# Kernel tuning notes

Measured on AMD Instinct MI355X. Metric: run time of the kernel, lower is better.

Reference implementation:

```python
import jax, jax.numpy as jnp
import numpy as np

N, E = 50000, 800000          # nodes, edges
H, C = 4, 64                  # heads, out_channels
F_IN, F_E = 5, 1              # node feature dim, edge feature dim
NEG_SLOPE = 0.2               # PyG GATConv default LeakyReLU slope
EPS = 1e-16                   # PyG softmax denominator epsilon


def setup_inputs() -> dict:
    key = jax.random.key(0)
    ks = jax.random.split(key, 10)
    return {
        "x": jax.random.normal(ks[0], (N, F_IN), jnp.float32),
        "edge_attr": jax.random.normal(ks[1], (E, F_E), jnp.float32),
        "u": jax.random.normal(ks[2], (1, 1), jnp.float32),
        # learned params (glorot-ish scale)
        "W": jax.random.normal(ks[3], (F_IN, H * C), jnp.float32) * 0.3,
        "W_edge": jax.random.normal(ks[4], (F_E, H * C), jnp.float32) * 0.3,
        "att_src": jax.random.normal(ks[5], (H, C), jnp.float32) * 0.1,
        "att_dst": jax.random.normal(ks[6], (H, C), jnp.float32) * 0.1,
        "att_edge": jax.random.normal(ks[7], (H, C), jnp.float32) * 0.1,
        "bias": jnp.zeros((C,), jnp.float32),
        "edge_index": jax.random.randint(ks[8], (2, E), 0, N, dtype=jnp.int32),
        "batch": jnp.zeros((N,), jnp.int32),
    }


def reference(x, edge_attr, u, W, W_edge, att_src, att_dst, att_edge, bias,
              edge_index, batch):
    # dropout p=0.0 is identity; u and batch are unused by the module's forward.
    src, dst = edge_index[0], edge_index[1]

    # node transform: [N, H, C]
    h = (x @ W).reshape(-1, H, C)
    # per-node attention logits: [N, H]
    a_src = jnp.einsum("nhc,hc->nh", h, att_src)
    a_dst = jnp.einsum("nhc,hc->nh", h, att_dst)

    # edge transform + edge attention logits: [E, H]
    e = (edge_attr @ W_edge).reshape(-1, H, C)
    a_edge = jnp.einsum("ehc,hc->eh", e, att_edge)

    # per-edge logits, LeakyReLU: [E, H]
    alpha = jax.nn.leaky_relu(a_src[src] + a_dst[dst] + a_edge, NEG_SLOPE)

    # segment softmax grouped by destination node
    m = jax.ops.segment_max(alpha, dst, num_segments=N)        # [N, H]
    alpha = jnp.exp(alpha - m[dst])
    s = jax.ops.segment_sum(alpha, dst, num_segments=N)        # [N, H]
    alpha = alpha / (s[dst] + EPS)

    # weighted scatter-aggregate of source features: [N, H, C]
    msg = h[src] * alpha[:, :, None]                           # [E, H, C]
    out = jax.ops.segment_sum(msg, dst, num_segments=N)

    # concat=False -> mean over heads, then bias: [N, C]
    return out.mean(axis=1) + bias
```

## Files before the change

kernel.cpp:

```cpp
#include <hip/hip_runtime.h>
#include <hip/hip_fp16.h>

#define N_NODES 50000
#define N_EDGES 800000
#define NH 4
#define NC 64
#define HC 256
#define F_IN 5
#define NEG_SLOPE 0.2f
#define SM_EPS 1e-16f
#define CAP 64
#define EPT 4
#define NPB 64
#define PREP_BLOCKS ((N_NODES + 255) / 256)
#define PLACE_BLOCKS ((N_EDGES + 256 * EPT - 1) / (256 * EPT))
#define GO_GRID ((N_NODES + NPB - 1) / NPB)

__device__ __forceinline__ float wave_reduce_sum(float v) {
#pragma unroll
    for (int o = 32; o > 0; o >>= 1) v += __shfl_xor(v, o, 64);
    return v;
}

__global__ __launch_bounds__(256) void prep_place_kernel(
        const float* __restrict__ x, const float* __restrict__ W,
        const float* __restrict__ att_src, const float* __restrict__ att_dst,
        const int* __restrict__ ei, const float* __restrict__ edge_attr,
        float* __restrict__ nrec, int* __restrict__ cursor,
        unsigned int* __restrict__ rec) {
    const int t = threadIdx.x;
    if (blockIdx.x < PREP_BLOCKS) {
        __shared__ float Vs[F_IN][NH], Vd[F_IN][NH];
        const int head = t >> 6, lane = t & 63;
        const float asv = att_src[t], adv = att_dst[t];
#pragma unroll
        for (int f = 0; f < F_IN; ++f) {
            const float w = W[f * HC + t];
            float vs = wave_reduce_sum(w * asv);
            float vd = wave_reduce_sum(w * adv);
            if (lane == 0) { Vs[f][head] = vs; Vd[f][head] = vd; }
        }
        __syncthreads();

        const int n = blockIdx.x * 256 + t;
        if (n >= N_NODES) return;
        float xs[F_IN];
#pragma unroll
        for (int f = 0; f < F_IN; ++f) xs[f] = x[n * F_IN + f];
        float as[NH] = {0.f, 0.f, 0.f, 0.f}, ad[NH] = {0.f, 0.f, 0.f, 0.f};
#pragma unroll
        for (int f = 0; f < F_IN; ++f)
#pragma unroll
            for (int h = 0; h < NH; ++h) {
                as[h] += xs[f] * Vs[f][h];
                ad[h] += xs[f] * Vd[f][h];
            }
        float* r = nrec + (size_t)n * 16;
        ((float4*)r)[0] = make_float4(as[0], as[1], as[2], as[3]);
        ((float4*)r)[1] = make_float4(xs[0], xs[1], xs[2], xs[3]);
        ((float4*)r)[2] = make_float4(xs[4], 0.f, 0.f, 0.f);
        ((float4*)r)[3] = make_float4(ad[0], ad[1], ad[2], ad[3]);
    } else {
        const int pb = blockIdx.x - PREP_BLOCKS;
        const int e0 = (pb * 256 + t) * EPT;
        if (e0 >= N_EDGES) return;
        if (e0 + EPT <= N_EDGES) {
            const int4 s4 = *(const int4*)(ei + e0);
            const int4 d4 = *(const int4*)(ei + N_EDGES + e0);
            const float4 a4 = *(const float4*)(edge_attr + e0);
            const int ss[EPT] = {s4.x, s4.y, s4.z, s4.w};
            const int dd[EPT] = {d4.x, d4.y, d4.z, d4.w};
            const float aa[EPT] = {a4.x, a4.y, a4.z, a4.w};
            int slot[EPT];
#pragma unroll
            for (int k = 0; k < EPT; ++k) slot[k] = atomicAdd(&cursor[dd[k]], 1);
#pragma unroll
            for (int k = 0; k < EPT; ++k) {
                if (slot[k] < CAP) {
                    const unsigned int h16 =
                        (unsigned int)__half_as_ushort(__float2half(aa[k]));
                    rec[(size_t)dd[k] * CAP + slot[k]] =
                        ((unsigned int)ss[k] << 16) | h16;
                }
            }
        } else {
            for (int e = e0; e < N_EDGES; ++e) {
                const int src = ei[e];
                const int dst = ei[N_EDGES + e];
                const int slot = atomicAdd(&cursor[dst], 1);
                if (slot < CAP) {
                    const unsigned int h16 =
                        (unsigned int)__half_as_ushort(__float2half(edge_attr[e]));
                    rec[(size_t)dst * CAP + slot] = ((unsigned int)src << 16) | h16;
                }
            }
        }
    }
}

__global__ __launch_bounds__(256) void gatherout_kernel(
        const float* __restrict__ W_edge, const float* __restrict__ att_edge,
        const int* __restrict__ cursor, const unsigned int* __restrict__ rec,
        const float* __restrict__ nrec, const float* __restrict__ W,
        const float* __restrict__ bias, float* __restrict__ out) {
    __shared__ float aeS[NH];
    __shared__ float nacc[NPB][21];
    const int t = threadIdx.x;
    {
        const int head = t >> 6, lane = t & 63;
        float v = wave_reduce_sum(W_edge[t] * att_edge[t]);
        if (lane == 0) aeS[head] = v;
    }
    __syncthreads();
    const float ae0 = aeS[0], ae1 = aeS[1], ae2 = aeS[2], ae3 = aeS[3];

    const int nl = t >> 2, parity = t & 3;
    const int n = blockIdx.x * NPB + nl;

    float acc[NH][F_IN];
#pragma unroll
    for (int h = 0; h < NH; ++h)
#pragma unroll
        for (int f = 0; f < F_IN; ++f) acc[h][f] = 0.f;
    float sden[NH] = {0.f, 0.f, 0.f, 0.f};

    if (n < N_NODES) {
        int cnt = cursor[n];
        cnt = cnt < CAP ? cnt : CAP;
        const float4 ad = ((const float4*)(nrec + (size_t)n * 16))[3];
        const unsigned int* rp = rec + (size_t)n * CAP;
        for (int i = parity; i < cnt; i += 4) {
            const unsigned int r = rp[i];
            const int src = (int)(r >> 16);
            const float ea = __half2float(__ushort_as_half((unsigned short)(r & 0xffffu)));
            const float* sr = nrec + (size_t)src * 16;
            const float4 as = ((const float4*)sr)[0];
            const float4 xa = ((const float4*)sr)[1];
            const float x4v = sr[8];
            float l0 = as.x + ad.x + ea * ae0;
            float l1 = as.y + ad.y + ea * ae1;
            float l2 = as.z + ad.z + ea * ae2;
            float l3 = as.w + ad.w + ea * ae3;
            l0 = l0 > 0.f ? l0 : NEG_SLOPE * l0;
            l1 = l1 > 0.f ? l1 : NEG_SLOPE * l1;
            l2 = l2 > 0.f ? l2 : NEG_SLOPE * l2;
            l3 = l3 > 0.f ? l3 : NEG_SLOPE * l3;
            const float p0 = expf(l0), p1 = expf(l1), p2 = expf(l2), p3 = expf(l3);
            const float xs[F_IN] = {xa.x, xa.y, xa.z, xa.w, x4v};
            const float pv[NH] = {p0, p1, p2, p3};
#pragma unroll
            for (int h = 0; h < NH; ++h) {
                sden[h] += pv[h];
#pragma unroll
                for (int f = 0; f < F_IN; ++f) acc[h][f] += pv[h] * xs[f];
            }
        }
    }
#pragma unroll
    for (int h = 0; h < NH; ++h) {
        sden[h] += __shfl_xor(sden[h], 1, 64);
        sden[h] += __shfl_xor(sden[h], 2, 64);
#pragma unroll
        for (int f = 0; f < F_IN; ++f) {
            acc[h][f] += __shfl_xor(acc[h][f], 1, 64);
            acc[h][f] += __shfl_xor(acc[h][f], 2, 64);
        }
    }
    if (parity == 0 && n < N_NODES) {
#pragma unroll
        for (int h = 0; h < NH; ++h) {
            const float is = 0.25f / (sden[h] + SM_EPS);
#pragma unroll
            for (int f = 0; f < F_IN; ++f) nacc[nl][h * F_IN + f] = acc[h][f] * is;
        }
    }
    __syncthreads();

    const int c = t & 63;
    float wreg[NH][F_IN];
#pragma unroll
    for (int h = 0; h < NH; ++h)
#pragma unroll
        for (int f = 0; f < F_IN; ++f) wreg[h][f] = W[f * HC + h * NC + c];
    const float bv = bias[c];
#pragma unroll
    for (int k = 0; k < NPB / 4; ++k) {
        const int nl2 = k * 4 + (t >> 6);
        const int n2 = blockIdx.x * NPB + nl2;
        if (n2 < N_NODES) {
            float r = bv;
#pragma unroll
            for (int h = 0; h < NH; ++h)
#pragma unroll
                for (int f = 0; f < F_IN; ++f)
                    r += nacc[nl2][h * F_IN + f] * wreg[h][f];
            out[(size_t)n2 * NC + c] = r;
        }
    }
}

extern "C" void kernel_launch(void* const* d_in, const int* in_sizes, int n_in,
                              void* d_out, int out_size, void* d_ws, size_t ws_size,
                              hipStream_t stream) {
    const float* x         = (const float*)d_in[0];
    const float* edge_attr = (const float*)d_in[1];
    const float* W         = (const float*)d_in[3];
    const float* W_edge    = (const float*)d_in[4];
    const float* att_src   = (const float*)d_in[5];
    const float* att_dst   = (const float*)d_in[6];
    const float* att_edge  = (const float*)d_in[7];
    const float* bias      = (const float*)d_in[8];
    const int*   ei        = (const int*)d_in[9];
    float* out = (float*)d_out;

    float* f = (float*)d_ws;
    size_t off = 0;
    float* nrec  = f + off; off += (size_t)N_NODES * 16;
    int* cursor  = (int*)(f + off); off += N_NODES;
    unsigned int* rec = (unsigned int*)(f + off);

    hipMemsetAsync(cursor, 0, N_NODES * sizeof(int), stream);
    prep_place_kernel<<<PREP_BLOCKS + PLACE_BLOCKS, 256, 0, stream>>>(
        x, W, att_src, att_dst, ei, edge_attr, nrec, cursor, rec);
    gatherout_kernel<<<GO_GRID, 256, 0, stream>>>(W_edge, att_edge, cursor, rec,
                                                  nrec, W, bias, out);
}
```

Baseline: 149.0 us.

## Pad edge cursors, split prep/place kernels, and vectorize record loads

Spaces the per-node atomic cursors 16 ints apart (64 bytes) so concurrent atomics on different destinations no longer share a cache line. The separate memset is replaced by zeroing the cursors inside a new prep kernel, which now runs as its own launch ahead of a dedicated place kernel. The gather loop reads four packed edge records at a time with one uint4 load. The trade-offs are a larger, sparser cursor array, an extra kernel launch, and serialization of prep and place that previously ran in one fused grid.

Result: slower. 162.5 us (+9.1%).

```diff
diff --git a/kernel.cpp b/kernel.cpp
--- a/kernel.cpp
+++ b/kernel.cpp
@@ -10,10 +10,11 @@
 #define NEG_SLOPE 0.2f
 #define SM_EPS 1e-16f
 #define CAP 64
+#define CSTRIDE 16
 #define EPT 4
 #define NPB 64
-#define PREP_BLOCKS ((N_NODES + 255) / 256)
-#define PLACE_BLOCKS ((N_EDGES + 256 * EPT - 1) / (256 * EPT))
+#define PREP_GRID ((N_NODES + 255) / 256)
+#define PLACE_GRID ((N_EDGES + 256 * EPT - 1) / (256 * EPT))
 #define GO_GRID ((N_NODES + NPB - 1) / NPB)
 
 __device__ __forceinline__ float wave_reduce_sum(float v) {
@@ -22,78 +23,65 @@
     return v;
 }
 
-__global__ __launch_bounds__(256) void prep_place_kernel(
+__global__ __launch_bounds__(256) void prep_kernel(
         const float* __restrict__ x, const float* __restrict__ W,
         const float* __restrict__ att_src, const float* __restrict__ att_dst,
+        float* __restrict__ nrec, int* __restrict__ cursor) {
+    __shared__ float Vs[F_IN][NH], Vd[F_IN][NH];
+    const int t = threadIdx.x;
+    const int head = t >> 6, lane = t & 63;
+    const float asv = att_src[t], adv = att_dst[t];
+#pragma unroll
+    for (int f = 0; f < F_IN; ++f) {
+        const float w = W[f * HC + t];
+        float vs = wave_reduce_sum(w * asv);
+        float vd = wave_reduce_sum(w * adv);
+        if (lane == 0) { Vs[f][head] = vs; Vd[f][head] = vd; }
+    }
+    __syncthreads();
+
+    const int n = blockIdx.x * 256 + t;
+    if (n >= N_NODES) return;
+    float xs[F_IN];
+#pragma unroll
+    for (int f = 0; f < F_IN; ++f) xs[f] = x[n * F_IN + f];
+    float as[NH] = {0.f, 0.f, 0.f, 0.f}, ad[NH] = {0.f, 0.f, 0.f, 0.f};
+#pragma unroll
+    for (int f = 0; f < F_IN; ++f)
+#pragma unroll
+        for (int h = 0; h < NH; ++h) {
+            as[h] += xs[f] * Vs[f][h];
+            ad[h] += xs[f] * Vd[f][h];
+        }
+    float* r = nrec + (size_t)n * 16;
+    ((float4*)r)[0] = make_float4(as[0], as[1], as[2], as[3]);
+    ((float4*)r)[1] = make_float4(xs[0], xs[1], xs[2], xs[3]);
+    ((float4*)r)[2] = make_float4(xs[4], 0.f, 0.f, 0.f);
+    ((float4*)r)[3] = make_float4(ad[0], ad[1], ad[2], ad[3]);
+    cursor[n * CSTRIDE] = 0;
+}
+
+__global__ __launch_bounds__(256) void place_kernel(
         const int* __restrict__ ei, const float* __restrict__ edge_attr,
-        float* __restrict__ nrec, int* __restrict__ cursor,
-        unsigned int* __restrict__ rec) {
-    const int t = threadIdx.x;
-    if (blockIdx.x < PREP_BLOCKS) {
-        __shared__ float Vs[F_IN][NH], Vd[F_IN][NH];
-        const int head = t >> 6, lane = t & 63;
-        const float asv = att_src[t], adv = att_dst[t];
-#pragma unroll
-        for (int f = 0; f < F_IN; ++f) {
-            const float w = W[f * HC + t];
-            float vs = wave_reduce_sum(w * asv);
-            float vd = wave_reduce_sum(w * adv);
-            if (lane == 0) { Vs[f][head] = vs; Vd[f][head] = vd; }
-        }
-        __syncthreads();
-
-        const int n = blockIdx.x * 256 + t;
-        if (n >= N_NODES) return;
-        float xs[F_IN];
-#pragma unroll
-        for (int f = 0; f < F_IN; ++f) xs[f] = x[n * F_IN + f];
-        float as[NH] = {0.f, 0.f, 0.f, 0.f}, ad[NH] = {0.f, 0.f, 0.f, 0.f};
-#pragma unroll
-        for (int f = 0; f < F_IN; ++f)
-#pragma unroll
-            for (int h = 0; h < NH; ++h) {
-                as[h] += xs[f] * Vs[f][h];
-                ad[h] += xs[f] * Vd[f][h];
-            }
-        float* r = nrec + (size_t)n * 16;
-        ((float4*)r)[0] = make_float4(as[0], as[1], as[2], as[3]);
-        ((float4*)r)[1] = make_float4(xs[0], xs[1], xs[2], xs[3]);
-        ((float4*)r)[2] = make_float4(xs[4], 0.f, 0.f, 0.f);
-        ((float4*)r)[3] = make_float4(ad[0], ad[1], ad[2], ad[3]);
-    } else {
-        const int pb = blockIdx.x - PREP_BLOCKS;
-        const int e0 = (pb * 256 + t) * EPT;
-        if (e0 >= N_EDGES) return;
-        if (e0 + EPT <= N_EDGES) {
-            const int4 s4 = *(const int4*)(ei + e0);
-            const int4 d4 = *(const int4*)(ei + N_EDGES + e0);
-            const float4 a4 = *(const float4*)(edge_attr + e0);
-            const int ss[EPT] = {s4.x, s4.y, s4.z, s4.w};
-            const int dd[EPT] = {d4.x, d4.y, d4.z, d4.w};
-            const float aa[EPT] = {a4.x, a4.y, a4.z, a4.w};
-            int slot[EPT];
-#pragma unroll
-            for (int k = 0; k < EPT; ++k) slot[k] = atomicAdd(&cursor[dd[k]], 1);
-#pragma unroll
-            for (int k = 0; k < EPT; ++k) {
-                if (slot[k] < CAP) {
-                    const unsigned int h16 =
-                        (unsigned int)__half_as_ushort(__float2half(aa[k]));
-                    rec[(size_t)dd[k] * CAP + slot[k]] =
-                        ((unsigned int)ss[k] << 16) | h16;
-                }
-            }
-        } else {
-            for (int e = e0; e < N_EDGES; ++e) {
-                const int src = ei[e];
-                const int dst = ei[N_EDGES + e];
-                const int slot = atomicAdd(&cursor[dst], 1);
-                if (slot < CAP) {
-                    const unsigned int h16 =
-                        (unsigned int)__half_as_ushort(__float2half(edge_attr[e]));
-                    rec[(size_t)dst * CAP + slot] = ((unsigned int)src << 16) | h16;
-                }
-            }
+        int* __restrict__ cursor, unsigned int* __restrict__ rec) {
+    const int e0 = (blockIdx.x * 256 + threadIdx.x) * EPT;
+    if (e0 >= N_EDGES) return;
+    const int4 s4 = *(const int4*)(ei + e0);
+    const int4 d4 = *(const int4*)(ei + N_EDGES + e0);
+    const float4 a4 = *(const float4*)(edge_attr + e0);
+    const int ss[EPT] = {s4.x, s4.y, s4.z, s4.w};
+    const int dd[EPT] = {d4.x, d4.y, d4.z, d4.w};
+    const float aa[EPT] = {a4.x, a4.y, a4.z, a4.w};
+    int slot[EPT];
+#pragma unroll
+    for (int k = 0; k < EPT; ++k)
+        slot[k] = atomicAdd(&cursor[dd[k] * CSTRIDE], 1);
+#pragma unroll
+    for (int k = 0; k < EPT; ++k) {
+        if (slot[k] < CAP) {
+            const unsigned int h16 =
+                (unsigned int)__half_as_ushort(__float2half(aa[k]));
+            rec[(size_t)dd[k] * CAP + slot[k]] = ((unsigned int)ss[k] << 16) | h16;
         }
     }
 }
@@ -125,34 +113,45 @@
     float sden[NH] = {0.f, 0.f, 0.f, 0.f};
 
     if (n < N_NODES) {
-        int cnt = cursor[n];
+        int cnt = cursor[n * CSTRIDE];
         cnt = cnt < CAP ? cnt : CAP;
         const float4 ad = ((const float4*)(nrec + (size_t)n * 16))[3];
         const unsigned int* rp = rec + (size_t)n * CAP;
-        for (int i = parity; i < cnt; i += 4) {
-            const unsigned int r = rp[i];
-            const int src = (int)(r >> 16);
-            const float ea = __half2float(__ushort_as_half((unsigned short)(r & 0xffffu)));
-            const float* sr = nrec + (size_t)src * 16;
-            const float4 as = ((const float4*)sr)[0];
-            const float4 xa = ((const float4*)sr)[1];
-            const float x4v = sr[8];
-            float l0 = as.x + ad.x + ea * ae0;
-            float l1 = as.y + ad.y + ea * ae1;
-            float l2 = as.z + ad.z + ea * ae2;
-            float l3 = as.w + ad.w + ea * ae3;
-            l0 = l0 > 0.f ? l0 : NEG_SLOPE * l0;
-            l1 = l1 > 0.f ? l1 : NEG_SLOPE * l1;
-            l2 = l2 > 0.f ? l2 : NEG_SLOPE * l2;
-            l3 = l3 > 0.f ? l3 : NEG_SLOPE * l3;
-            const float p0 = expf(l0), p1 = expf(l1), p2 = expf(l2), p3 = expf(l3);
-            const float xs[F_IN] = {xa.x, xa.y, xa.z, xa.w, x4v};
-            const float pv[NH] = {p0, p1, p2, p3};
-#pragma unroll
-            for (int h = 0; h < NH; ++h) {
-                sden[h] += pv[h];
-#pragma unroll
-                for (int f = 0; f < F_IN; ++f) acc[h][f] += pv[h] * xs[f];
+        for (int j = 0; j * 16 < cnt; ++j) {
+            const int base = j * 16 + parity * 4;
+            uint r4[4];
+            *(uint4*)r4 = *(const uint4*)(rp + base);
+#pragma unroll
+            for (int k = 0; k < 4; ++k) {
+                const int idx = base + k;
+                if (idx < cnt) {
+                    const unsigned int r = r4[k];
+                    const int src = (int)(r >> 16);
+                    const float ea = __half2float(
+                        __ushort_as_half((unsigned short)(r & 0xffffu)));
+                    const float* sr = nrec + (size_t)src * 16;
+                    const float4 as = ((const float4*)sr)[0];
+                    const float4 xa = ((const float4*)sr)[1];
+                    const float x4v = sr[8];
+                    float l0 = as.x + ad.x + ea * ae0;
+                    float l1 = as.y + ad.y + ea * ae1;
+                    float l2 = as.z + ad.z + ea * ae2;
+                    float l3 = as.w + ad.w + ea * ae3;
+                    l0 = l0 > 0.f ? l0 : NEG_SLOPE * l0;
+                    l1 = l1 > 0.f ? l1 : NEG_SLOPE * l1;
+                    l2 = l2 > 0.f ? l2 : NEG_SLOPE * l2;
+                    l3 = l3 > 0.f ? l3 : NEG_SLOPE * l3;
+                    const float p0 = expf(l0), p1 = expf(l1);
+                    const float p2 = expf(l2), p3 = expf(l3);
+                    const float xs[F_IN] = {xa.x, xa.y, xa.z, xa.w, x4v};
+                    const float pv[NH] = {p0, p1, p2, p3};
+#pragma unroll
+                    for (int h = 0; h < NH; ++h) {
+                        sden[h] += pv[h];
+#pragma unroll
+                        for (int f = 0; f < F_IN; ++f) acc[h][f] += pv[h] * xs[f];
+                    }
+                }
             }
         }
     }
@@ -216,12 +215,12 @@
     float* f = (float*)d_ws;
     size_t off = 0;
     float* nrec  = f + off; off += (size_t)N_NODES * 16;
-    int* cursor  = (int*)(f + off); off += N_NODES;
+    int* cursor  = (int*)(f + off); off += (size_t)N_NODES * CSTRIDE;
     unsigned int* rec = (unsigned int*)(f + off);
 
-    hipMemsetAsync(cursor, 0, N_NODES * sizeof(int), stream);
-    prep_place_kernel<<<PREP_BLOCKS + PLACE_BLOCKS, 256, 0, stream>>>(
-        x, W, att_src, att_dst, ei, edge_attr, nrec, cursor, rec);
+    prep_kernel<<<PREP_GRID, 256, 0, stream>>>(x, W, att_src, att_dst,
+                                               nrec, cursor);
+    place_kernel<<<PLACE_GRID, 256, 0, stream>>>(ei, edge_attr, cursor, rec);
     gatherout_kernel<<<GO_GRID, 256, 0, stream>>>(W_edge, att_edge, cursor, rec,
                                                   nrec, W, bias, out);
 }
```
